# Optimization experiments

Measured on AMD Instinct MI355X. Metric: run time of the kernel, lower is better.

Reference implementation:

```python
import jax, jax.numpy as jnp
import numpy as np

NUM_USER = 100000
NUM_ENT = 200000
NUM_REL = 32
DIM = 64
N_NEIGHBOR = 16
BATCH = 16384


def setup_inputs() -> dict:
    key = jax.random.key(0)
    ks = jax.random.split(key, 11)
    inp = {
        "u": jax.random.randint(ks[0], (BATCH,), 0, NUM_USER),
        "v": jax.random.randint(ks[1], (BATCH,), 0, NUM_ENT),
        "user_neighbor": jax.random.randint(ks[2], (BATCH, N_NEIGHBOR), 0, NUM_ENT),
        "item_neighbor": jax.random.randint(ks[3], (BATCH, N_NEIGHBOR), 0, NUM_USER),
        "adj_ent": jax.random.randint(ks[4], (NUM_ENT, N_NEIGHBOR), 0, NUM_ENT),
        "adj_rel": jax.random.randint(ks[5], (NUM_ENT, N_NEIGHBOR), 0, NUM_REL),
        "usr_emb": jax.random.normal(ks[6], (NUM_USER, DIM), dtype=jnp.float32) * 0.1,
        "ent_emb": jax.random.normal(ks[7], (NUM_ENT, DIM), dtype=jnp.float32) * 0.1,
        "rel_emb": jax.random.normal(ks[8], (NUM_REL, DIM), dtype=jnp.float32) * 0.1,
        "agg_W": jax.random.normal(ks[9], (DIM, DIM), dtype=jnp.float32) * (1.0 / np.sqrt(DIM)),
        "agg_b": jax.random.normal(ks[10], (DIM,), dtype=jnp.float32) * 0.01,
    }
    return inp


def reference(u, v, user_neighbor, item_neighbor, adj_ent, adj_rel,
              usr_emb, ent_emb, rel_emb, agg_W, agg_b):
    n = N_NEIGHBOR
    # LightGCN-style "lite" embeddings: mean over sampled interaction neighbors
    lite_user = usr_emb[item_neighbor].sum(axis=1) * (1.0 / n)   # [B, D]
    lite_item = ent_emb[user_neighbor].sum(axis=1) * (1.0 / n)   # [B, D]

    user_embeddings = usr_emb[u]                                  # [B, D]
    item_embeddings_original = ent_emb[v]                         # [B, D]

    # one-hop KG neighbors of items
    nbr_ent = adj_ent[v]                                          # [B, n]
    nbr_rel = adj_rel[v]                                          # [B, n]
    self_vectors = item_embeddings_original[:, None, :]           # [B, 1, D]
    neighbor_vectors = ent_emb[nbr_ent][:, None, :, :]            # [B, 1, n, D]
    neighbor_relations = rel_emb[nbr_rel][:, None, :, :]          # [B, 1, n, D]

    # KGCN sum-aggregator: user-relation attention over neighbors
    ur_scores = jnp.einsum("bd,bknd->bkn", user_embeddings, neighbor_relations)
    attn = jax.nn.softmax(ur_scores, axis=-1)                     # [B, 1, n]
    neighbors_agg = jnp.einsum("bkn,bknd->bkd", attn, neighbor_vectors)
    combined = self_vectors + neighbors_agg                       # [B, 1, D]
    item_embeddings = jnp.tanh(combined @ agg_W + agg_b)[:, 0, :]  # [B, D]

    user_final = 0.5 * lite_user + 0.5 * user_embeddings
    item_final = 0.5 * lite_item + 0.5 * item_embeddings
    scores = jnp.sum(user_final * item_final, axis=1)
    return jax.nn.sigmoid(scores)
```

## Files before the change

### kernel.cpp

```cpp
#include <hip/hip_runtime.h>
#include <math.h>

#define DIM 64
#define NNB 16
#define BATCH 16384

typedef float4 f4;

__device__ __forceinline__ float dot4(const f4 a, const f4 b) {
    return fmaf(a.x, b.x, fmaf(a.y, b.y, fmaf(a.z, b.z, a.w * b.w)));
}

__device__ __forceinline__ f4 xgrp_sum(f4 v) {
    v.x += __shfl_xor(v.x, 16, 64); v.y += __shfl_xor(v.y, 16, 64);
    v.z += __shfl_xor(v.z, 16, 64); v.w += __shfl_xor(v.w, 16, 64);
    v.x += __shfl_xor(v.x, 32, 64); v.y += __shfl_xor(v.y, 32, 64);
    v.z += __shfl_xor(v.z, 32, 64); v.w += __shfl_xor(v.w, 32, 64);
    return v;
}

template <int WPB>
__global__ __launch_bounds__(WPB * 64, 4) void klgcn_kernel(
    const int* __restrict__ u, const int* __restrict__ v,
    const int* __restrict__ user_neighbor, const int* __restrict__ item_neighbor,
    const int* __restrict__ adj_ent, const int* __restrict__ adj_rel,
    const float* __restrict__ usr_emb, const float* __restrict__ ent_emb,
    const float* __restrict__ rel_emb, const float* __restrict__ agg_W,
    const float* __restrict__ agg_b, float* __restrict__ out)
{
    const int wave = threadIdx.x >> 6;
    const int lane = threadIdx.x & 63;
    const int g = lane >> 4;
    const int s = lane & 15;
    const int b = __builtin_amdgcn_readfirstlane(blockIdx.x * WPB + wave);

    const f4* __restrict__ usr4 = (const f4*)usr_emb;
    const f4* __restrict__ ent4 = (const f4*)ent_emb;
    const f4* __restrict__ rel4 = (const f4*)rel_emb;
    const f4* __restrict__ W4   = (const f4*)agg_W;
    const f4* __restrict__ b4p  = (const f4*)agg_b;

    const int ub = __builtin_amdgcn_readfirstlane(u[b]);
    const int vb = __builtin_amdgcn_readfirstlane(v[b]);

    int i_it[NNB], i_un[NNB], i_ar[NNB], i_ae[NNB];
#pragma unroll
    for (int n = 0; n < NNB; n++)
        i_it[n] = __builtin_amdgcn_readfirstlane(item_neighbor[b * NNB + n]);
#pragma unroll
    for (int n = 0; n < NNB; n++)
        i_un[n] = __builtin_amdgcn_readfirstlane(user_neighbor[b * NNB + n]);
#pragma unroll
    for (int n = 0; n < NNB; n++)
        i_ar[n] = __builtin_amdgcn_readfirstlane(adj_rel[vb * NNB + n]);
#pragma unroll
    for (int n = 0; n < NNB; n++)
        i_ae[n] = __builtin_amdgcn_readfirstlane(adj_ent[vb * NNB + n]);

    f4 ue4 = usr4[(long)ub * 16 + s];
    f4 ie4 = ent4[(long)vb * 16 + s];
    f4 Re[4], Ag[4], Lu[4], Li[4];
#pragma unroll
    for (int k = 0; k < 4; k++) Re[k] = rel4[i_ar[4 * k + g] * 16 + s];
#pragma unroll
    for (int k = 0; k < 4; k++) Ag[k] = ent4[(long)i_ae[4 * k + g] * 16 + s];
#pragma unroll
    for (int k = 0; k < 4; k++) Lu[k] = usr4[(long)i_it[4 * k + g] * 16 + s];
#pragma unroll
    for (int k = 0; k < 4; k++) Li[k] = ent4[(long)i_un[4 * k + g] * 16 + s];

    float sc[4];
#pragma unroll
    for (int k = 0; k < 4; k++) {
        float p = dot4(ue4, Re[k]);
        p += __shfl_xor(p, 1, 64); p += __shfl_xor(p, 2, 64);
        p += __shfl_xor(p, 4, 64); p += __shfl_xor(p, 8, 64);
        sc[k] = p;
    }
    float m = fmaxf(fmaxf(sc[0], sc[1]), fmaxf(sc[2], sc[3]));
    m = fmaxf(m, __shfl_xor(m, 16, 64));
    m = fmaxf(m, __shfl_xor(m, 32, 64));
    float e[4];
    float ssum = 0.f;
#pragma unroll
    for (int k = 0; k < 4; k++) { e[k] = __expf(sc[k] - m); ssum += e[k]; }
    ssum += __shfl_xor(ssum, 16, 64);
    ssum += __shfl_xor(ssum, 32, 64);
    const float inv = 1.0f / ssum;

    f4 ag = {0.f, 0.f, 0.f, 0.f};
#pragma unroll
    for (int k = 0; k < 4; k++) {
        ag.x = fmaf(e[k], Ag[k].x, ag.x);
        ag.y = fmaf(e[k], Ag[k].y, ag.y);
        ag.z = fmaf(e[k], Ag[k].z, ag.z);
        ag.w = fmaf(e[k], Ag[k].w, ag.w);
    }
    ag = xgrp_sum(ag);

    f4 comb;
    comb.x = fmaf(ag.x, inv, ie4.x);
    comb.y = fmaf(ag.y, inv, ie4.y);
    comb.z = fmaf(ag.z, inv, ie4.z);
    comb.w = fmaf(ag.w, inv, ie4.w);
    const float cc[4] = {comb.x, comb.y, comb.z, comb.w};

    f4 lu;
    lu.x = Lu[0].x + Lu[1].x + Lu[2].x + Lu[3].x;
    lu.y = Lu[0].y + Lu[1].y + Lu[2].y + Lu[3].y;
    lu.z = Lu[0].z + Lu[1].z + Lu[2].z + Lu[3].z;
    lu.w = Lu[0].w + Lu[1].w + Lu[2].w + Lu[3].w;
    lu = xgrp_sum(lu);
    f4 li;
    li.x = Li[0].x + Li[1].x + Li[2].x + Li[3].x;
    li.y = Li[0].y + Li[1].y + Li[2].y + Li[3].y;
    li.z = Li[0].z + Li[1].z + Li[2].z + Li[3].z;
    li.w = Li[0].w + Li[1].w + Li[2].w + Li[3].w;
    li = xgrp_sum(li);

    f4 acc = {0.f, 0.f, 0.f, 0.f};
#pragma unroll
    for (int j = 0; j < 16; j++) {
        const int d = 16 * g + j;
        const float cd = __shfl(cc[j & 3], 20 * g + (j >> 2), 64);
        const f4 w = W4[d * 16 + s];
        acc.x = fmaf(cd, w.x, acc.x);
        acc.y = fmaf(cd, w.y, acc.y);
        acc.z = fmaf(cd, w.z, acc.z);
        acc.w = fmaf(cd, w.w, acc.w);
    }
    acc = xgrp_sum(acc);
    const f4 bias = b4p[s];
    f4 item4;
    item4.x = tanhf(acc.x + bias.x);
    item4.y = tanhf(acc.y + bias.y);
    item4.z = tanhf(acc.z + bias.z);
    item4.w = tanhf(acc.w + bias.w);

    f4 uf, itf;
    uf.x = 0.5f * fmaf(lu.x, 1.f / NNB, ue4.x);
    uf.y = 0.5f * fmaf(lu.y, 1.f / NNB, ue4.y);
    uf.z = 0.5f * fmaf(lu.z, 1.f / NNB, ue4.z);
    uf.w = 0.5f * fmaf(lu.w, 1.f / NNB, ue4.w);
    itf.x = 0.5f * fmaf(li.x, 1.f / NNB, item4.x);
    itf.y = 0.5f * fmaf(li.y, 1.f / NNB, item4.y);
    itf.z = 0.5f * fmaf(li.z, 1.f / NNB, item4.z);
    itf.w = 0.5f * fmaf(li.w, 1.f / NNB, item4.w);

    float p = dot4(uf, itf);
    p += __shfl_xor(p, 1, 64); p += __shfl_xor(p, 2, 64);
    p += __shfl_xor(p, 4, 64); p += __shfl_xor(p, 8, 64);

    if (lane == 0) out[b] = 1.0f / (1.0f + __expf(-p));
}

extern "C" void kernel_launch(void* const* d_in, const int* in_sizes, int n_in,
                              void* d_out, int out_size, void* d_ws, size_t ws_size,
                              hipStream_t stream)
{
    const int*   u             = (const int*)d_in[0];
    const int*   v             = (const int*)d_in[1];
    const int*   user_neighbor = (const int*)d_in[2];
    const int*   item_neighbor = (const int*)d_in[3];
    const int*   adj_ent       = (const int*)d_in[4];
    const int*   adj_rel       = (const int*)d_in[5];
    const float* usr_emb       = (const float*)d_in[6];
    const float* ent_emb       = (const float*)d_in[7];
    const float* rel_emb       = (const float*)d_in[8];
    const float* agg_W         = (const float*)d_in[9];
    const float* agg_b         = (const float*)d_in[10];
    float* out = (float*)d_out;

    constexpr int WPB = 4;
    dim3 grid(BATCH / WPB), block(WPB * 64);
    klgcn_kernel<WPB><<<grid, block, 0, stream>>>(
        u, v, user_neighbor, item_neighbor, adj_ent, adj_rel,
        usr_emb, ent_emb, rel_emb, agg_W, agg_b, out);
}
```

Baseline: 178.1 us.

## Process two batch rows per wave with vectorized per-lane index loads

After: 150.8 us. 1.18x faster.

```diff
diff --git a/kernel.cpp b/kernel.cpp
--- a/kernel.cpp
+++ b/kernel.cpp
@@ -20,7 +20,7 @@
 }
 
 template <int WPB>
-__global__ __launch_bounds__(WPB * 64, 4) void klgcn_kernel(
+__global__ __launch_bounds__(WPB * 64, 3) void klgcn_kernel(
     const int* __restrict__ u, const int* __restrict__ v,
     const int* __restrict__ user_neighbor, const int* __restrict__ item_neighbor,
     const int* __restrict__ adj_ent, const int* __restrict__ adj_rel,
@@ -32,126 +32,173 @@
     const int lane = threadIdx.x & 63;
     const int g = lane >> 4;
     const int s = lane & 15;
-    const int b = __builtin_amdgcn_readfirstlane(blockIdx.x * WPB + wave);
+    const int b0 = __builtin_amdgcn_readfirstlane((blockIdx.x * WPB + wave) * 2);
+    const int bb[2] = {b0, b0 + 1};
 
     const f4* __restrict__ usr4 = (const f4*)usr_emb;
     const f4* __restrict__ ent4 = (const f4*)ent_emb;
     const f4* __restrict__ rel4 = (const f4*)rel_emb;
     const f4* __restrict__ W4   = (const f4*)agg_W;
     const f4* __restrict__ b4p  = (const f4*)agg_b;
-
-    const int ub = __builtin_amdgcn_readfirstlane(u[b]);
-    const int vb = __builtin_amdgcn_readfirstlane(v[b]);
-
-    int i_it[NNB], i_un[NNB], i_ar[NNB], i_ae[NNB];
-#pragma unroll
-    for (int n = 0; n < NNB; n++)
-        i_it[n] = __builtin_amdgcn_readfirstlane(item_neighbor[b * NNB + n]);
-#pragma unroll
-    for (int n = 0; n < NNB; n++)
-        i_un[n] = __builtin_amdgcn_readfirstlane(user_neighbor[b * NNB + n]);
-#pragma unroll
-    for (int n = 0; n < NNB; n++)
-        i_ar[n] = __builtin_amdgcn_readfirstlane(adj_rel[vb * NNB + n]);
-#pragma unroll
-    for (int n = 0; n < NNB; n++)
-        i_ae[n] = __builtin_amdgcn_readfirstlane(adj_ent[vb * NNB + n]);
-
-    f4 ue4 = usr4[(long)ub * 16 + s];
-    f4 ie4 = ent4[(long)vb * 16 + s];
-    f4 Re[4], Ag[4], Lu[4], Li[4];
-#pragma unroll
-    for (int k = 0; k < 4; k++) Re[k] = rel4[i_ar[4 * k + g] * 16 + s];
-#pragma unroll
-    for (int k = 0; k < 4; k++) Ag[k] = ent4[(long)i_ae[4 * k + g] * 16 + s];
-#pragma unroll
-    for (int k = 0; k < 4; k++) Lu[k] = usr4[(long)i_it[4 * k + g] * 16 + s];
-#pragma unroll
-    for (int k = 0; k < 4; k++) Li[k] = ent4[(long)i_un[4 * k + g] * 16 + s];
-
-    float sc[4];
-#pragma unroll
-    for (int k = 0; k < 4; k++) {
-        float p = dot4(ue4, Re[k]);
+    const int4* __restrict__ it4 = (const int4*)item_neighbor;
+    const int4* __restrict__ un4 = (const int4*)user_neighbor;
+    const int4* __restrict__ ar4 = (const int4*)adj_rel;
+    const int4* __restrict__ ae4 = (const int4*)adj_ent;
+
+    int ub[2], vb[2];
+#pragma unroll
+    for (int el = 0; el < 2; el++) {
+        ub[el] = __builtin_amdgcn_readfirstlane(u[bb[el]]);
+        vb[el] = __builtin_amdgcn_readfirstlane(v[bb[el]]);
+    }
+
+    int4 iit[2], iun[2], iar[2], iae[2];
+#pragma unroll
+    for (int el = 0; el < 2; el++) {
+        iit[el] = it4[bb[el] * 4 + g];
+        iun[el] = un4[bb[el] * 4 + g];
+        iar[el] = ar4[vb[el] * 4 + g];
+        iae[el] = ae4[vb[el] * 4 + g];
+    }
+
+    f4 ue4[2], ie4[2];
+#pragma unroll
+    for (int el = 0; el < 2; el++) {
+        ue4[el] = usr4[(long)ub[el] * 16 + s];
+        ie4[el] = ent4[(long)vb[el] * 16 + s];
+    }
+
+    f4 Re[2][4], Ag[2][4], Lu[2][4], Li[2][4];
+#pragma unroll
+    for (int el = 0; el < 2; el++) {
+        Re[el][0] = rel4[iar[el].x * 16 + s];
+        Re[el][1] = rel4[iar[el].y * 16 + s];
+        Re[el][2] = rel4[iar[el].z * 16 + s];
+        Re[el][3] = rel4[iar[el].w * 16 + s];
+    }
+#pragma unroll
+    for (int el = 0; el < 2; el++) {
+        Ag[el][0] = ent4[(long)iae[el].x * 16 + s];
+        Ag[el][1] = ent4[(long)iae[el].y * 16 + s];
+        Ag[el][2] = ent4[(long)iae[el].z * 16 + s];
+        Ag[el][3] = ent4[(long)iae[el].w * 16 + s];
+    }
+#pragma unroll
+    for (int el = 0; el < 2; el++) {
+        Lu[el][0] = usr4[(long)iit[el].x * 16 + s];
+        Lu[el][1] = usr4[(long)iit[el].y * 16 + s];
+        Lu[el][2] = usr4[(long)iit[el].z * 16 + s];
+        Lu[el][3] = usr4[(long)iit[el].w * 16 + s];
+    }
+#pragma unroll
+    for (int el = 0; el < 2; el++) {
+        Li[el][0] = ent4[(long)iun[el].x * 16 + s];
+        Li[el][1] = ent4[(long)iun[el].y * 16 + s];
+        Li[el][2] = ent4[(long)iun[el].z * 16 + s];
+        Li[el][3] = ent4[(long)iun[el].w * 16 + s];
+    }
+
+    float e[2][4], inv[2];
+#pragma unroll
+    for (int el = 0; el < 2; el++) {
+        float sc[4];
+#pragma unroll
+        for (int k = 0; k < 4; k++) {
+            float p = dot4(ue4[el], Re[el][k]);
+            p += __shfl_xor(p, 1, 64); p += __shfl_xor(p, 2, 64);
+            p += __shfl_xor(p, 4, 64); p += __shfl_xor(p, 8, 64);
+            sc[k] = p;
+        }
+        float m = fmaxf(fmaxf(sc[0], sc[1]), fmaxf(sc[2], sc[3]));
+        m = fmaxf(m, __shfl_xor(m, 16, 64));
+        m = fmaxf(m, __shfl_xor(m, 32, 64));
+        float ssum = 0.f;
+#pragma unroll
+        for (int k = 0; k < 4; k++) { e[el][k] = __expf(sc[k] - m); ssum += e[el][k]; }
+        ssum += __shfl_xor(ssum, 16, 64);
+        ssum += __shfl_xor(ssum, 32, 64);
+        inv[el] = 1.0f / ssum;
+    }
+
+    float cc[2][4];
+#pragma unroll
+    for (int el = 0; el < 2; el++) {
+        f4 ag = {0.f, 0.f, 0.f, 0.f};
+#pragma unroll
+        for (int k = 0; k < 4; k++) {
+            ag.x = fmaf(e[el][k], Ag[el][k].x, ag.x);
+            ag.y = fmaf(e[el][k], Ag[el][k].y, ag.y);
+            ag.z = fmaf(e[el][k], Ag[el][k].z, ag.z);
+            ag.w = fmaf(e[el][k], Ag[el][k].w, ag.w);
+        }
+        ag = xgrp_sum(ag);
+        cc[el][0] = fmaf(ag.x, inv[el], ie4[el].x);
+        cc[el][1] = fmaf(ag.y, inv[el], ie4[el].y);
+        cc[el][2] = fmaf(ag.z, inv[el], ie4[el].z);
+        cc[el][3] = fmaf(ag.w, inv[el], ie4[el].w);
+    }
+
+    f4 lu[2], li[2];
+#pragma unroll
+    for (int el = 0; el < 2; el++) {
+        f4 t;
+        t.x = Lu[el][0].x + Lu[el][1].x + Lu[el][2].x + Lu[el][3].x;
+        t.y = Lu[el][0].y + Lu[el][1].y + Lu[el][2].y + Lu[el][3].y;
+        t.z = Lu[el][0].z + Lu[el][1].z + Lu[el][2].z + Lu[el][3].z;
+        t.w = Lu[el][0].w + Lu[el][1].w + Lu[el][2].w + Lu[el][3].w;
+        lu[el] = xgrp_sum(t);
+        t.x = Li[el][0].x + Li[el][1].x + Li[el][2].x + Li[el][3].x;
+        t.y = Li[el][0].y + Li[el][1].y + Li[el][2].y + Li[el][3].y;
+        t.z = Li[el][0].z + Li[el][1].z + Li[el][2].z + Li[el][3].z;
+        t.w = Li[el][0].w + Li[el][1].w + Li[el][2].w + Li[el][3].w;
+        li[el] = xgrp_sum(t);
+    }
+
+    f4 acc[2] = {{0.f, 0.f, 0.f, 0.f}, {0.f, 0.f, 0.f, 0.f}};
+#pragma unroll
+    for (int j = 0; j < 16; j++) {
+        const int d = 16 * g + j;
+        const f4 w = W4[d * 16 + s];
+        const int src = 20 * g + (j >> 2);
+#pragma unroll
+        for (int el = 0; el < 2; el++) {
+            const float cd = __shfl(cc[el][j & 3], src, 64);
+            acc[el].x = fmaf(cd, w.x, acc[el].x);
+            acc[el].y = fmaf(cd, w.y, acc[el].y);
+            acc[el].z = fmaf(cd, w.z, acc[el].z);
+            acc[el].w = fmaf(cd, w.w, acc[el].w);
+        }
+    }
+    const f4 bias = b4p[s];
+    float res[2];
+#pragma unroll
+    for (int el = 0; el < 2; el++) {
+        acc[el] = xgrp_sum(acc[el]);
+        f4 item4;
+        item4.x = tanhf(acc[el].x + bias.x);
+        item4.y = tanhf(acc[el].y + bias.y);
+        item4.z = tanhf(acc[el].z + bias.z);
+        item4.w = tanhf(acc[el].w + bias.w);
+
+        f4 uf, itf;
+        uf.x = 0.5f * fmaf(lu[el].x, 1.f / NNB, ue4[el].x);
+        uf.y = 0.5f * fmaf(lu[el].y, 1.f / NNB, ue4[el].y);
+        uf.z = 0.5f * fmaf(lu[el].z, 1.f / NNB, ue4[el].z);
+        uf.w = 0.5f * fmaf(lu[el].w, 1.f / NNB, ue4[el].w);
+        itf.x = 0.5f * fmaf(li[el].x, 1.f / NNB, item4.x);
+        itf.y = 0.5f * fmaf(li[el].y, 1.f / NNB, item4.y);
+        itf.z = 0.5f * fmaf(li[el].z, 1.f / NNB, item4.z);
+        itf.w = 0.5f * fmaf(li[el].w, 1.f / NNB, item4.w);
+
+        float p = dot4(uf, itf);
         p += __shfl_xor(p, 1, 64); p += __shfl_xor(p, 2, 64);
         p += __shfl_xor(p, 4, 64); p += __shfl_xor(p, 8, 64);
-        sc[k] = p;
-    }
-    float m = fmaxf(fmaxf(sc[0], sc[1]), fmaxf(sc[2], sc[3]));
-    m = fmaxf(m, __shfl_xor(m, 16, 64));
-    m = fmaxf(m, __shfl_xor(m, 32, 64));
-    float e[4];
-    float ssum = 0.f;
-#pragma unroll
-    for (int k = 0; k < 4; k++) { e[k] = __expf(sc[k] - m); ssum += e[k]; }
-    ssum += __shfl_xor(ssum, 16, 64);
-    ssum += __shfl_xor(ssum, 32, 64);
-    const float inv = 1.0f / ssum;
-
-    f4 ag = {0.f, 0.f, 0.f, 0.f};
-#pragma unroll
-    for (int k = 0; k < 4; k++) {
-        ag.x = fmaf(e[k], Ag[k].x, ag.x);
-        ag.y = fmaf(e[k], Ag[k].y, ag.y);
-        ag.z = fmaf(e[k], Ag[k].z, ag.z);
-        ag.w = fmaf(e[k], Ag[k].w, ag.w);
-    }
-    ag = xgrp_sum(ag);
-
-    f4 comb;
-    comb.x = fmaf(ag.x, inv, ie4.x);
-    comb.y = fmaf(ag.y, inv, ie4.y);
-    comb.z = fmaf(ag.z, inv, ie4.z);
-    comb.w = fmaf(ag.w, inv, ie4.w);
-    const float cc[4] = {comb.x, comb.y, comb.z, comb.w};
-
-    f4 lu;
-    lu.x = Lu[0].x + Lu[1].x + Lu[2].x + Lu[3].x;
-    lu.y = Lu[0].y + Lu[1].y + Lu[2].y + Lu[3].y;
-    lu.z = Lu[0].z + Lu[1].z + Lu[2].z + Lu[3].z;
-    lu.w = Lu[0].w + Lu[1].w + Lu[2].w + Lu[3].w;
-    lu = xgrp_sum(lu);
-    f4 li;
-    li.x = Li[0].x + Li[1].x + Li[2].x + Li[3].x;
-    li.y = Li[0].y + Li[1].y + Li[2].y + Li[3].y;
-    li.z = Li[0].z + Li[1].z + Li[2].z + Li[3].z;
-    li.w = Li[0].w + Li[1].w + Li[2].w + Li[3].w;
-    li = xgrp_sum(li);
-
-    f4 acc = {0.f, 0.f, 0.f, 0.f};
-#pragma unroll
-    for (int j = 0; j < 16; j++) {
-        const int d = 16 * g + j;
-        const float cd = __shfl(cc[j & 3], 20 * g + (j >> 2), 64);
-        const f4 w = W4[d * 16 + s];
-        acc.x = fmaf(cd, w.x, acc.x);
-        acc.y = fmaf(cd, w.y, acc.y);
-        acc.z = fmaf(cd, w.z, acc.z);
-        acc.w = fmaf(cd, w.w, acc.w);
-    }
-    acc = xgrp_sum(acc);
-    const f4 bias = b4p[s];
-    f4 item4;
-    item4.x = tanhf(acc.x + bias.x);
-    item4.y = tanhf(acc.y + bias.y);
-    item4.z = tanhf(acc.z + bias.z);
-    item4.w = tanhf(acc.w + bias.w);
-
-    f4 uf, itf;
-    uf.x = 0.5f * fmaf(lu.x, 1.f / NNB, ue4.x);
-    uf.y = 0.5f * fmaf(lu.y, 1.f / NNB, ue4.y);
-    uf.z = 0.5f * fmaf(lu.z, 1.f / NNB, ue4.z);
-    uf.w = 0.5f * fmaf(lu.w, 1.f / NNB, ue4.w);
-    itf.x = 0.5f * fmaf(li.x, 1.f / NNB, item4.x);
-    itf.y = 0.5f * fmaf(li.y, 1.f / NNB, item4.y);
-    itf.z = 0.5f * fmaf(li.z, 1.f / NNB, item4.z);
-    itf.w = 0.5f * fmaf(li.w, 1.f / NNB, item4.w);
-
-    float p = dot4(uf, itf);
-    p += __shfl_xor(p, 1, 64); p += __shfl_xor(p, 2, 64);
-    p += __shfl_xor(p, 4, 64); p += __shfl_xor(p, 8, 64);
-
-    if (lane == 0) out[b] = 1.0f / (1.0f + __expf(-p));
+        res[el] = 1.0f / (1.0f + __expf(-p));
+    }
+
+    if (lane == 0) {
+        *(float2*)(out + b0) = make_float2(res[0], res[1]);
+    }
 }
 
 extern "C" void kernel_launch(void* const* d_in, const int* in_sizes, int n_in,
@@ -172,7 +219,7 @@
     float* out = (float*)d_out;
 
     constexpr int WPB = 4;
-    dim3 grid(BATCH / WPB), block(WPB * 64);
+    dim3 grid(BATCH / (WPB * 2)), block(WPB * 64);
     klgcn_kernel<WPB><<<grid, block, 0, stream>>>(
         u, v, user_neighbor, item_neighbor, adj_ent, adj_rel,
         usr_emb, ent_emb, rel_emb, agg_W, agg_b, out);
```
